# Performance work log

Hardware: AMD Instinct MI355X
Metric: run time of the kernel (lower is better)

The kernel has to match this reference:

```python
import jax, jax.numpy as jnp
import numpy as np

B, N = 16, 128
DN0, DE0, DH = 64, 16, 128  # input node dim, input edge dim, hidden dim


def _gnn2(A, x, e, w_msg, b_msg, w_node, b_node):
    """One GNN2 layer on dense batched graphs.
    A: [B,N,N] adjacency mask, x: [B,N,Dn], e: [B,N,N,De].
    Message/new-edge: relu(Linear([x_i, x_j, e_ij])) masked by A.
    New node: relu(Linear([x, sum_j msg_ij])).
    The concat-Linear is decomposed into three matmuls to avoid
    materializing the [B,N,N,2Dn+De] concat tensor.
    """
    Dn = x.shape[-1]
    Wi, Wj, We = w_msg[:Dn], w_msg[Dn:2 * Dn], w_msg[2 * Dn:]
    xi = x @ Wi                                   # [B,N,Do]
    xj = x @ Wj                                   # [B,N,Do]
    msg = jax.nn.relu(xi[:, :, None, :] + xj[:, None, :, :] + e @ We + b_msg)
    msg = msg * A[..., None]                      # mask non-edges -> new edge_attr [B,N,N,Do]
    agg = msg.sum(axis=2)                         # scatter-sum over neighbors j -> [B,N,Do]
    Wx, Wa = w_node[:Dn], w_node[Dn:]
    x_new = jax.nn.relu(x @ Wx + agg @ Wa + b_node)
    return x_new, msg


def setup_inputs() -> dict:
    key = jax.random.key(0)
    ks = iter(jax.random.split(key, 32))
    s = 0.05
    inp = {
        "edge_index": jax.random.randint(next(ks), (B, N, N), 0, 2, dtype=jnp.int32),
        "x": jax.random.normal(next(ks), (B, N, DN0), dtype=jnp.float32),
        "edge_attr": jax.random.normal(next(ks), (B, N, N, DE0), dtype=jnp.float32),
    }
    def w(shape):
        return s * jax.random.normal(next(ks), shape, dtype=jnp.float32)
    # layer 0: node_in=64, edge_in=16 -> 128
    inp["w_msg_0"], inp["b_msg_0"] = w((2 * DN0 + DE0, DH)), w((DH,))
    inp["w_node_0"], inp["b_node_0"] = w((DN0 + DH, DH)), w((DH,))
    # layers 1,2: 128 -> 128
    for l in (1, 2):
        inp[f"w_msg_{l}"], inp[f"b_msg_{l}"] = w((2 * DH + DH, DH)), w((DH,))
        inp[f"w_node_{l}"], inp[f"b_node_{l}"] = w((DH + DH, DH)), w((DH,))
    # head mlp: 128 -> 128 -> 128 -> 1
    inp["w_h1"], inp["b_h1"] = w((DH, DH)), w((DH,))
    inp["w_h2"], inp["b_h2"] = w((DH, DH)), w((DH,))
    inp["w_h3"], inp["b_h3"] = w((DH, 1)), w((1,))
    return inp


def reference(edge_index, x, edge_attr,
              w_msg_0, b_msg_0, w_node_0, b_node_0,
              w_msg_1, b_msg_1, w_node_1, b_node_1,
              w_msg_2, b_msg_2, w_node_2, b_node_2,
              w_h1, b_h1, w_h2, b_h2, w_h3, b_h3):
    A = edge_index.astype(jnp.float32)
    x = x.astype(jnp.float32)
    # layer 0
    x, e = _gnn2(A, x, edge_attr, w_msg_0, b_msg_0, w_node_0, b_node_0)
    # middle layer with 0.5 residual blend
    x_, e_ = _gnn2(A, x, e, w_msg_1, b_msg_1, w_node_1, b_node_1)
    x = 0.5 * (x + x_)
    e = 0.5 * (e + e_)
    # last layer
    x, e = _gnn2(A, x, e, w_msg_2, b_msg_2, w_node_2, b_node_2)
    # edge_mean readout + MLP head
    h = e.mean(axis=(1, 2))                       # [B, DH]
    h = jax.nn.relu(h @ w_h1 + b_h1)
    h = jax.nn.relu(h @ w_h2 + b_h2)
    out = h @ w_h3 + b_h3                         # [B, 1]
    return out.squeeze(-1)                        # [B]
```

## Files before the change

kernel.cpp:

```cpp
#include <hip/hip_runtime.h>

constexpr int B = 16, N = 128, D = 128, DN0 = 64, DE0 = 16;

typedef _Float16 half8 __attribute__((ext_vector_type(8)));
typedef _Float16 half4 __attribute__((ext_vector_type(4)));
typedef float floatx4 __attribute__((ext_vector_type(4)));

__device__ __forceinline__ void gld16(const _Float16* g, _Float16* l) {
  __builtin_amdgcn_global_load_lds(
      (const __attribute__((address_space(1))) void*)g,
      (__attribute__((address_space(3))) void*)l, 16, 0, 0);
}

__global__ __launch_bounds__(128) void k_wprep(
    const float* __restrict__ wm1, const float* __restrict__ wm2,
    _Float16* __restrict__ weT1, _Float16* __restrict__ weT2) {
  const int bid = blockIdx.x;
  const int layer = bid >> 7, c = bid & 127;
  const int k = threadIdx.x;
  const float* src = layer ? wm2 : wm1;
  _Float16* dst = layer ? weT2 : weT1;
  dst[c * D + k] = (_Float16)src[(2 * D + k) * D + c];
}

__global__ __launch_bounds__(128) void k_pre0(
    const float* __restrict__ x, const float* __restrict__ wm0,
    const float* __restrict__ bm0,
    float* __restrict__ xi0, float* __restrict__ xj0) {
  const int row = blockIdx.x;
  const int c = threadIdx.x;
  __shared__ float xr[DN0];
  if (c < DN0) xr[c] = x[row * DN0 + c];
  __syncthreads();
  float ai = bm0[c], aj = 0.f;
  #pragma unroll 8
  for (int k = 0; k < DN0; ++k) {
    const float xv = xr[k];
    ai = fmaf(xv, wm0[k * D + c], ai);
    aj = fmaf(xv, wm0[(DN0 + k) * D + c], aj);
  }
  xi0[row * D + c] = ai;
  xj0[row * D + c] = aj;
}

__global__ __launch_bounds__(256) void k_edge0(
    const int* __restrict__ ei, const float* __restrict__ eattr,
    const float* __restrict__ wm0,
    const float* __restrict__ xi0, const float* __restrict__ xj0,
    _Float16* __restrict__ msg0, float* __restrict__ agg0) {
  const int row = blockIdx.x;
  const int b = row >> 7;
  const int t = threadIdx.x;
  const int c4 = (t & 31) * 4, jb = t >> 5;

  __shared__ float e_row[N][20];
  __shared__ float w_t[DE0][D];
  __shared__ float amask[N];
  __shared__ float xi_r[D];
  __shared__ float hp2[8][32][4];

  const float4* esrc = (const float4*)(eattr + (size_t)row * N * DE0);
  const float4* wsrc = (const float4*)(wm0 + 2 * DN0 * D);
  #pragma unroll
  for (int u = 0; u < 2; ++u) {
    const int idx4 = u * 256 + t;
    const int j = idx4 >> 2;
    const int k4 = (idx4 & 3) * 4;
    *(float4*)&e_row[j][k4] = esrc[idx4];
    ((float4*)&w_t[0][0])[idx4] = wsrc[idx4];
  }
  if (t < N) {
    amask[t] = (float)ei[(size_t)row * N + t];
    xi_r[t] = xi0[row * D + t];
  }
  __syncthreads();

  float acc[16][4] = {};
  #pragma unroll 4
  for (int k = 0; k < DE0; ++k) {
    float av[16];
    #pragma unroll
    for (int p = 0; p < 16; ++p) av[p] = e_row[jb + 8 * p][k];
    const floatx4 wv = *(const floatx4*)&w_t[k][c4];
    #pragma unroll
    for (int p = 0; p < 16; ++p)
      #pragma unroll
      for (int q = 0; q < 4; ++q)
        acc[p][q] = fmaf(av[p], wv[q], acc[p][q]);
  }

  float hq[4] = {};
  const float* xjb = xj0 + (size_t)b * N * D;
  _Float16* mrow = msg0 + (size_t)row * N * D;
  const floatx4 xiv = *(const floatx4*)&xi_r[c4];
  #pragma unroll
  for (int p = 0; p < 16; ++p) {
    const int j = jb + 8 * p;
    const float am = amask[j];
    const floatx4 xjv = *(const floatx4*)&xjb[j * D + c4];
    half4 hv;
    #pragma unroll
    for (int q = 0; q < 4; ++q) {
      float v = xiv[q] + xjv[q] + acc[p][q];
      v = fmaxf(v, 0.f) * am;
      hv[q] = (_Float16)v;
      hq[q] += v;
    }
    const int cell = (c4 >> 3) ^ (j & 15);
    *(half4*)&mrow[j * D + cell * 8 + (c4 & 7)] = hv;
  }
  #pragma unroll
  for (int q = 0; q < 4; ++q) hp2[jb][t & 31][q] = hq[q];
  __syncthreads();
  if (t < D) {
    float s = 0.f;
    #pragma unroll
    for (int g = 0; g < 8; ++g) s += hp2[g][t >> 2][t & 3];
    agg0[row * D + t] = s;
  }
}

__global__ __launch_bounds__(128) void k_node0(
    const float* __restrict__ x0, const float* __restrict__ agg0,
    const float* __restrict__ wn0, const float* __restrict__ bn0,
    const float* __restrict__ wm1, const float* __restrict__ bm1,
    float* __restrict__ x1, float* __restrict__ xi1, float* __restrict__ xj1) {
  const int row = blockIdx.x;
  const int c = threadIdx.x;
  __shared__ float xr[DN0], ar[D], x1r[D];
  if (c < DN0) xr[c] = x0[row * DN0 + c];
  ar[c] = agg0[row * D + c];
  __syncthreads();
  float a = bn0[c];
  #pragma unroll 8
  for (int k = 0; k < DN0; ++k) a = fmaf(xr[k], wn0[k * D + c], a);
  #pragma unroll 8
  for (int k = 0; k < D; ++k) a = fmaf(ar[k], wn0[(DN0 + k) * D + c], a);
  a = fmaxf(a, 0.f);
  x1[row * D + c] = a;
  x1r[c] = a;
  __syncthreads();
  float ai = bm1[c], aj = 0.f;
  #pragma unroll 8
  for (int k = 0; k < D; ++k) {
    const float xv = x1r[k];
    ai = fmaf(xv, wm1[k * D + c], ai);
    aj = fmaf(xv, wm1[(D + k) * D + c], aj);
  }
  xi1[row * D + c] = ai;
  xj1[row * D + c] = aj;
}

__global__ __launch_bounds__(128) void k_node1(
    const float* __restrict__ x1, const float* __restrict__ agg1,
    const float* __restrict__ wn1, const float* __restrict__ bn1,
    const float* __restrict__ wm2, const float* __restrict__ bm2,
    float* __restrict__ xi2, float* __restrict__ xj2) {
  const int row = blockIdx.x;
  const int c = threadIdx.x;
  __shared__ float x1r[D], ar[D], x2r[D];
  x1r[c] = x1[row * D + c];
  ar[c] = agg1[row * D + c];
  __syncthreads();
  float a = bn1[c];
  #pragma unroll 8
  for (int k = 0; k < D; ++k) a = fmaf(x1r[k], wn1[k * D + c], a);
  #pragma unroll 8
  for (int k = 0; k < D; ++k) a = fmaf(ar[k], wn1[(D + k) * D + c], a);
  x2r[c] = 0.5f * (x1r[c] + fmaxf(a, 0.f));
  __syncthreads();
  float ai = bm2[c], aj = 0.f;
  #pragma unroll 8
  for (int k = 0; k < D; ++k) {
    const float xv = x2r[k];
    ai = fmaf(xv, wm2[k * D + c], ai);
    aj = fmaf(xv, wm2[(D + k) * D + c], aj);
  }
  xi2[row * D + c] = ai;
  xj2[row * D + c] = aj;
}

__global__ __launch_bounds__(512, 4) void k_mid(
    const int* __restrict__ ei, const _Float16* __restrict__ weT1,
    const _Float16* __restrict__ weT2,
    const float* __restrict__ xi, const float* __restrict__ xj,
    _Float16* __restrict__ em,
    float* __restrict__ agg1) {
  const int row = blockIdx.x;
  const int b = row >> 7;
  const int t = threadIdx.x;
  const int w = t >> 6;
  const int lane = t & 63;
  const int lm = lane & 15, lq = lane >> 4;

  __shared__ _Float16 sE[N * D];

  half8 a1[4];
  #pragma unroll
  for (int ks = 0; ks < 4; ++ks)
    a1[ks] = *(const half8*)(weT1 + (16 * w + lm) * D + 8 * lq + 32 * ks);

  const _Float16* gsrc = em + (size_t)row * N * D;
  #pragma unroll
  for (int u = 0; u < 4; ++u) {
    const int seg = (u * 8 + w) * 512;
    gld16(gsrc + seg + lane * 8, &sE[seg]);
  }

  const int c0 = 16 * w + 4 * lq;
  const floatx4 xiv = *(const floatx4*)&xi[(size_t)row * D + c0];
  float am[8];
  #pragma unroll
  for (int jt = 0; jt < 8; ++jt)
    am[jt] = (float)ei[(size_t)row * N + 16 * jt + lm];

  __syncthreads();

  floatx4 acc[8];
  #pragma unroll
  for (int jt = 0; jt < 8; ++jt) acc[jt] = (floatx4){0.f, 0.f, 0.f, 0.f};
  #pragma unroll
  for (int ks = 0; ks < 4; ++ks)
    #pragma unroll
    for (int jt = 0; jt < 8; ++jt) {
      const half8 bv = *(const half8*)&sE[(16 * jt + lm) * D + (((lq + 4 * ks) ^ lm) << 3)];
      acc[jt] = __builtin_amdgcn_mfma_f32_16x16x32_f16(a1[ks], bv, acc[jt], 0, 0, 0);
    }

  __syncthreads();

  const float* xjb = xj + (size_t)b * N * D;
  floatx4 hacc = (floatx4){0.f, 0.f, 0.f, 0.f};
  #pragma unroll
  for (int jt = 0; jt < 8; ++jt) {
    const int j = 16 * jt + lm;
    const int hidx = j * D + (((2 * w + (lq >> 1)) ^ lm) << 3) + 4 * (lq & 1);
    const floatx4 xjv = *(const floatx4*)&xjb[j * D + c0];
    const half4 m0 = *(const half4*)&sE[hidx];
    half4 mid;
    floatx4 m1;
    #pragma unroll
    for (int r = 0; r < 4; ++r) {
      const float v = xiv[r] + xjv[r] + acc[jt][r];
      m1[r] = fmaxf(v, 0.f) * am[jt];
      mid[r] = (_Float16)(0.5f * ((float)m0[r] + m1[r]));
    }
    *(half4*)&sE[hidx] = mid;
    hacc += m1;
  }

  half8 a2[4];
  #pragma unroll
  for (int ks = 0; ks < 4; ++ks)
    a2[ks] = *(const half8*)(weT2 + (16 * w + lm) * D + 8 * lq + 32 * ks);

  __syncthreads();

  #pragma unroll
  for (int jt = 0; jt < 8; ++jt) acc[jt] = (floatx4){0.f, 0.f, 0.f, 0.f};
  #pragma unroll
  for (int ks = 0; ks < 4; ++ks)
    #pragma unroll
    for (int jt = 0; jt < 8; ++jt) {
      const half8 bv = *(const half8*)&sE[(16 * jt + lm) * D + (((lq + 4 * ks) ^ lm) << 3)];
      acc[jt] = __builtin_amdgcn_mfma_f32_16x16x32_f16(a2[ks], bv, acc[jt], 0, 0, 0);
    }

  #pragma unroll
  for (int m = 1; m < 16; m <<= 1)
    #pragma unroll
    for (int r = 0; r < 4; ++r)
      hacc[r] += __shfl_xor(hacc[r], m, 64);
  if (lm == 0)
    *(floatx4*)&agg1[(size_t)row * D + c0] = hacc;

  __syncthreads();

  #pragma unroll
  for (int jt = 0; jt < 8; ++jt) {
    const int j = 16 * jt + lm;
    const int hidx = j * D + (((2 * w + (lq >> 1)) ^ lm) << 3) + 4 * (lq & 1);
    half4 tv;
    #pragma unroll
    for (int r = 0; r < 4; ++r) tv[r] = (_Float16)acc[jt][r];
    *(half4*)&sE[hidx] = tv;
  }

  __syncthreads();

  uint4* gdst = (uint4*)(em + (size_t)row * N * D);
  const uint4* ls = (const uint4*)sE;
  #pragma unroll
  for (int u = 0; u < 4; ++u) {
    const int idx4 = (u * 8 + w) * 64 + lane;
    gdst[idx4] = ls[idx4];
  }
}

__global__ __launch_bounds__(256) void k_fin(
    const int* __restrict__ ei, const _Float16* __restrict__ t2,
    const float* __restrict__ xi, const float* __restrict__ xj,
    float* __restrict__ rowsum) {
  const int row = blockIdx.x;
  const int b = row >> 7;
  const int t = threadIdx.x;
  const int c8 = (t & 15) * 8, jr = t >> 4;

  __shared__ float sMask[N];
  __shared__ float hp[16][16][8];
  if (t < N) sMask[t] = (float)ei[(size_t)row * N + t];
  float xiv[8];
  *(floatx4*)&xiv[0] = *(const floatx4*)&xi[row * D + c8];
  *(floatx4*)&xiv[4] = *(const floatx4*)&xi[row * D + c8 + 4];
  __syncthreads();

  const _Float16* src = t2 + (size_t)row * N * D;
  const float* xjb = xj + (size_t)b * N * D;
  float acc8[8] = {};
  #pragma unroll
  for (int u = 0; u < 8; ++u) {
    const int j = u * 16 + jr;
    const half8 tv = *(const half8*)(src + j * D + (((t & 15) ^ jr) << 3));
    const float am = sMask[j];
    const floatx4 xj0 = *(const floatx4*)&xjb[j * D + c8];
    const floatx4 xj1 = *(const floatx4*)&xjb[j * D + c8 + 4];
    #pragma unroll
    for (int r = 0; r < 4; ++r) {
      acc8[r]     += fmaxf(xiv[r] + xj0[r] + (float)tv[r], 0.f) * am;
      acc8[4 + r] += fmaxf(xiv[4 + r] + xj1[r] + (float)tv[4 + r], 0.f) * am;
    }
  }
  #pragma unroll
  for (int k = 0; k < 8; ++k) hp[jr][t & 15][k] = acc8[k];
  __syncthreads();
  if (t < D) {
    float s = 0.f;
    #pragma unroll
    for (int g = 0; g < 16; ++g) s += hp[g][t >> 3][t & 7];
    rowsum[row * D + t] = s;
  }
}

__global__ __launch_bounds__(128) void k_head(
    const float* __restrict__ rowsum,
    const float* __restrict__ w1, const float* __restrict__ b1,
    const float* __restrict__ w2, const float* __restrict__ b2,
    const float* __restrict__ w3, const float* __restrict__ b3,
    float* __restrict__ out) {
  const int b = blockIdx.x;
  const int c = threadIdx.x;
  __shared__ float hr[D], h1r[D], h2r[D];
  const float* rs = rowsum + (size_t)b * N * D;
  float s = 0.f;
  for (int i = 0; i < N; ++i) s += rs[i * D + c];
  hr[c] = s * (1.f / (N * N));
  __syncthreads();
  float a = b1[c];
  #pragma unroll 8
  for (int k = 0; k < D; ++k) a = fmaf(hr[k], w1[k * D + c], a);
  h1r[c] = fmaxf(a, 0.f);
  __syncthreads();
  a = b2[c];
  #pragma unroll 8
  for (int k = 0; k < D; ++k) a = fmaf(h1r[k], w2[k * D + c], a);
  h2r[c] = fmaxf(a, 0.f);
  __syncthreads();
  hr[c] = h2r[c] * w3[c];
  __syncthreads();
  if (c == 0) {
    float s2 = b3[0];
    for (int k = 0; k < D; ++k) s2 += hr[k];
    out[b] = s2;
  }
}

extern "C" void kernel_launch(void* const* d_in, const int* in_sizes, int n_in,
                              void* d_out, int out_size, void* d_ws, size_t ws_size,
                              hipStream_t stream) {
  const int*   ei  = (const int*)d_in[0];
  const float* x0  = (const float*)d_in[1];
  const float* ea  = (const float*)d_in[2];
  const float* wm0 = (const float*)d_in[3];
  const float* bm0 = (const float*)d_in[4];
  const float* wn0 = (const float*)d_in[5];
  const float* bn0 = (const float*)d_in[6];
  const float* wm1 = (const float*)d_in[7];
  const float* bm1 = (const float*)d_in[8];
  const float* wn1 = (const float*)d_in[9];
  const float* bn1 = (const float*)d_in[10];
  const float* wm2 = (const float*)d_in[11];
  const float* bm2 = (const float*)d_in[12];
  const float* wh1 = (const float*)d_in[15];
  const float* bh1 = (const float*)d_in[16];
  const float* wh2 = (const float*)d_in[17];
  const float* bh2 = (const float*)d_in[18];
  const float* wh3 = (const float*)d_in[19];
  const float* bh3 = (const float*)d_in[20];
  float* out = (float*)d_out;

  _Float16* msg0h = (_Float16*)d_ws;
  _Float16* weT1  = msg0h + (size_t)B * N * N * D;
  _Float16* weT2  = weT1 + D * D;
  float* f = (float*)(weT2 + D * D);
  size_t off = 0;
  const size_t R = (size_t)B * N * D;
  float* xi0  = f + off; off += R;
  float* xj0  = f + off; off += R;
  float* agg0 = f + off; off += R;
  float* x1   = f + off; off += R;
  float* xi1  = f + off; off += R;
  float* xj1  = f + off; off += R;
  float* agg1 = f + off; off += R;
  float* xi2  = f + off; off += R;
  float* xj2  = f + off; off += R;
  float* rsum = f + off; off += R;

  const int rows = B * N;
  k_wprep<<<256, 128, 0, stream>>>(wm1, wm2, weT1, weT2);
  k_pre0 <<<rows, 128, 0, stream>>>(x0, wm0, bm0, xi0, xj0);
  k_edge0<<<rows, 256, 0, stream>>>(ei, ea, wm0, xi0, xj0, msg0h, agg0);
  k_node0<<<rows, 128, 0, stream>>>(x0, agg0, wn0, bn0, wm1, bm1, x1, xi1, xj1);
  k_mid  <<<rows, 512, 0, stream>>>(ei, weT1, weT2, xi1, xj1, msg0h, agg1);
  k_node1<<<rows, 128, 0, stream>>>(x1, agg1, wn1, bn1, wm2, bm2, xi2, xj2);
  k_fin  <<<rows, 256, 0, stream>>>(ei, msg0h, xi2, xj2, rsum);
  k_head <<<B,    128, 0, stream>>>(rsum, wh1, bh1, wh2, bh2, wh3, bh3, out);
}
```

Baseline: 240.7 us.

## Switch k_mid to 32x32x16 MFMA tiles with 4 waves per block

```diff
diff --git a/kernel.cpp b/kernel.cpp
--- a/kernel.cpp
+++ b/kernel.cpp
@@ -5,6 +5,7 @@
 typedef _Float16 half8 __attribute__((ext_vector_type(8)));
 typedef _Float16 half4 __attribute__((ext_vector_type(4)));
 typedef float floatx4 __attribute__((ext_vector_type(4)));
+typedef float floatx16 __attribute__((ext_vector_type(16)));
 
 __device__ __forceinline__ void gld16(const _Float16* g, _Float16* l) {
   __builtin_amdgcn_global_load_lds(
@@ -180,7 +181,7 @@
   xj2[row * D + c] = aj;
 }
 
-__global__ __launch_bounds__(512, 4) void k_mid(
+__global__ __launch_bounds__(256, 2) void k_mid(
     const int* __restrict__ ei, const _Float16* __restrict__ weT1,
     const _Float16* __restrict__ weT2,
     const float* __restrict__ xi, const float* __restrict__ xj,
@@ -191,99 +192,121 @@
   const int t = threadIdx.x;
   const int w = t >> 6;
   const int lane = t & 63;
-  const int lm = lane & 15, lq = lane >> 4;
+  const int l31 = lane & 31;
+  const int l15 = lane & 15;
+  const int hl = lane >> 5;
 
   __shared__ _Float16 sE[N * D];
 
-  half8 a1[4];
-  #pragma unroll
-  for (int ks = 0; ks < 4; ++ks)
-    a1[ks] = *(const half8*)(weT1 + (16 * w + lm) * D + 8 * lq + 32 * ks);
-
   const _Float16* gsrc = em + (size_t)row * N * D;
   #pragma unroll
-  for (int u = 0; u < 4; ++u) {
-    const int seg = (u * 8 + w) * 512;
+  for (int u = 0; u < 8; ++u) {
+    const int seg = (u * 4 + w) * 512;
     gld16(gsrc + seg + lane * 8, &sE[seg]);
   }
 
-  const int c0 = 16 * w + 4 * lq;
-  const floatx4 xiv = *(const floatx4*)&xi[(size_t)row * D + c0];
-  float am[8];
-  #pragma unroll
-  for (int jt = 0; jt < 8; ++jt)
-    am[jt] = (float)ei[(size_t)row * N + 16 * jt + lm];
-
-  __syncthreads();
-
-  floatx4 acc[8];
-  #pragma unroll
-  for (int jt = 0; jt < 8; ++jt) acc[jt] = (floatx4){0.f, 0.f, 0.f, 0.f};
-  #pragma unroll
-  for (int ks = 0; ks < 4; ++ks)
-    #pragma unroll
-    for (int jt = 0; jt < 8; ++jt) {
-      const half8 bv = *(const half8*)&sE[(16 * jt + lm) * D + (((lq + 4 * ks) ^ lm) << 3)];
-      acc[jt] = __builtin_amdgcn_mfma_f32_16x16x32_f16(a1[ks], bv, acc[jt], 0, 0, 0);
+  half8 a1[8];
+  #pragma unroll
+  for (int ks = 0; ks < 8; ++ks)
+    a1[ks] = *(const half8*)(weT1 + (32 * w + l31) * D + 16 * ks + 8 * hl);
+
+  floatx4 xiv[4];
+  #pragma unroll
+  for (int g = 0; g < 4; ++g)
+    xiv[g] = *(const floatx4*)&xi[(size_t)row * D + 32 * w + 8 * g + 4 * hl];
+  float am[4];
+  #pragma unroll
+  for (int jt = 0; jt < 4; ++jt)
+    am[jt] = (float)ei[(size_t)row * N + 32 * jt + l31];
+
+  __syncthreads();
+
+  const floatx16 vzero = {0.f,0.f,0.f,0.f,0.f,0.f,0.f,0.f,
+                          0.f,0.f,0.f,0.f,0.f,0.f,0.f,0.f};
+  floatx16 acc[4];
+  #pragma unroll
+  for (int jt = 0; jt < 4; ++jt) acc[jt] = vzero;
+  #pragma unroll
+  for (int ks = 0; ks < 8; ++ks)
+    #pragma unroll
+    for (int jt = 0; jt < 4; ++jt) {
+      const half8 bv = *(const half8*)
+          &sE[(32 * jt + l31) * D + (((2 * ks + hl) ^ l15) << 3)];
+      acc[jt] = __builtin_amdgcn_mfma_f32_32x32x16_f16(a1[ks], bv, acc[jt], 0, 0, 0);
     }
 
   __syncthreads();
 
   const float* xjb = xj + (size_t)b * N * D;
-  floatx4 hacc = (floatx4){0.f, 0.f, 0.f, 0.f};
-  #pragma unroll
-  for (int jt = 0; jt < 8; ++jt) {
-    const int j = 16 * jt + lm;
-    const int hidx = j * D + (((2 * w + (lq >> 1)) ^ lm) << 3) + 4 * (lq & 1);
-    const floatx4 xjv = *(const floatx4*)&xjb[j * D + c0];
-    const half4 m0 = *(const half4*)&sE[hidx];
-    half4 mid;
-    floatx4 m1;
-    #pragma unroll
-    for (int r = 0; r < 4; ++r) {
-      const float v = xiv[r] + xjv[r] + acc[jt][r];
-      m1[r] = fmaxf(v, 0.f) * am[jt];
-      mid[r] = (_Float16)(0.5f * ((float)m0[r] + m1[r]));
-    }
-    *(half4*)&sE[hidx] = mid;
-    hacc += m1;
-  }
-
-  half8 a2[4];
-  #pragma unroll
-  for (int ks = 0; ks < 4; ++ks)
-    a2[ks] = *(const half8*)(weT2 + (16 * w + lm) * D + 8 * lq + 32 * ks);
-
-  __syncthreads();
-
-  #pragma unroll
-  for (int jt = 0; jt < 8; ++jt) acc[jt] = (floatx4){0.f, 0.f, 0.f, 0.f};
-  #pragma unroll
-  for (int ks = 0; ks < 4; ++ks)
-    #pragma unroll
-    for (int jt = 0; jt < 8; ++jt) {
-      const half8 bv = *(const half8*)&sE[(16 * jt + lm) * D + (((lq + 4 * ks) ^ lm) << 3)];
-      acc[jt] = __builtin_amdgcn_mfma_f32_16x16x32_f16(a2[ks], bv, acc[jt], 0, 0, 0);
-    }
-
-  #pragma unroll
-  for (int m = 1; m < 16; m <<= 1)
-    #pragma unroll
-    for (int r = 0; r < 4; ++r)
-      hacc[r] += __shfl_xor(hacc[r], m, 64);
-  if (lm == 0)
-    *(floatx4*)&agg1[(size_t)row * D + c0] = hacc;
-
-  __syncthreads();
-
-  #pragma unroll
-  for (int jt = 0; jt < 8; ++jt) {
-    const int j = 16 * jt + lm;
-    const int hidx = j * D + (((2 * w + (lq >> 1)) ^ lm) << 3) + 4 * (lq & 1);
-    half4 tv;
-    #pragma unroll
-    for (int r = 0; r < 4; ++r) tv[r] = (_Float16)acc[jt][r];
-    *(half4*)&sE[hidx] = tv;
+  floatx4 hacc[4];
+  #pragma unroll
+  for (int g = 0; g < 4; ++g) hacc[g] = (floatx4){0.f, 0.f, 0.f, 0.f};
+  #pragma unroll
+  for (int jt = 0; jt < 4; ++jt) {
+    const int j = 32 * jt + l31;
+    #pragma unroll
+    for (int g = 0; g < 4; ++g) {
+      const int cofs = 32 * w + 8 * g + 4 * hl;
+      const int hidx = j * D + (((4 * w + g) ^ l15) << 3) + 4 * hl;
+      const floatx4 xjv = *(const floatx4*)&xjb[j * D + cofs];
+      const half4 m0 = *(const half4*)&sE[hidx];
+      half4 mid;
+      floatx4 m1;
+      #pragma unroll
+      for (int r = 0; r < 4; ++r) {
+        const float v = xiv[g][r] + xjv[r] + acc[jt][4 * g + r];
+        m1[r] = fmaxf(v, 0.f) * am[jt];
+        mid[r] = (_Float16)(0.5f * ((float)m0[r] + m1[r]));
+      }
+      *(half4*)&sE[hidx] = mid;
+      hacc[g] += m1;
+    }
+  }
+
+  #pragma unroll
+  for (int m = 1; m < 32; m <<= 1)
+    #pragma unroll
+    for (int g = 0; g < 4; ++g)
+      #pragma unroll
+      for (int r = 0; r < 4; ++r)
+        hacc[g][r] += __shfl_xor(hacc[g][r], m, 64);
+  if (l31 == 0) {
+    #pragma unroll
+    for (int g = 0; g < 4; ++g)
+      *(floatx4*)&agg1[(size_t)row * D + 32 * w + 8 * g + 4 * hl] = hacc[g];
+  }
+
+  half8 a2[8];
+  #pragma unroll
+  for (int ks = 0; ks < 8; ++ks)
+    a2[ks] = *(const half8*)(weT2 + (32 * w + l31) * D + 16 * ks + 8 * hl);
+
+  __syncthreads();
+
+  #pragma unroll
+  for (int jt = 0; jt < 4; ++jt) acc[jt] = vzero;
+  #pragma unroll
+  for (int ks = 0; ks < 8; ++ks)
+    #pragma unroll
+    for (int jt = 0; jt < 4; ++jt) {
+      const half8 bv = *(const half8*)
+          &sE[(32 * jt + l31) * D + (((2 * ks + hl) ^ l15) << 3)];
+      acc[jt] = __builtin_amdgcn_mfma_f32_32x32x16_f16(a2[ks], bv, acc[jt], 0, 0, 0);
+    }
+
+  __syncthreads();
+
+  #pragma unroll
+  for (int jt = 0; jt < 4; ++jt) {
+    const int j = 32 * jt + l31;
+    #pragma unroll
+    for (int g = 0; g < 4; ++g) {
+      const int hidx = j * D + (((4 * w + g) ^ l15) << 3) + 4 * hl;
+      half4 tv;
+      #pragma unroll
+      for (int r = 0; r < 4; ++r) tv[r] = (_Float16)acc[jt][4 * g + r];
+      *(half4*)&sE[hidx] = tv;
+    }
   }
 
   __syncthreads();
@@ -291,8 +314,8 @@
   uint4* gdst = (uint4*)(em + (size_t)row * N * D);
   const uint4* ls = (const uint4*)sE;
   #pragma unroll
-  for (int u = 0; u < 4; ++u) {
-    const int idx4 = (u * 8 + w) * 64 + lane;
+  for (int u = 0; u < 8; ++u) {
+    const int idx4 = u * 256 + t;
     gdst[idx4] = ls[idx4];
   }
 }
@@ -420,7 +443,7 @@
   k_pre0 <<<rows, 128, 0, stream>>>(x0, wm0, bm0, xi0, xj0);
   k_edge0<<<rows, 256, 0, stream>>>(ei, ea, wm0, xi0, xj0, msg0h, agg0);
   k_node0<<<rows, 128, 0, stream>>>(x0, agg0, wn0, bn0, wm1, bm1, x1, xi1, xj1);
-  k_mid  <<<rows, 512, 0, stream>>>(ei, weT1, weT2, xi1, xj1, msg0h, agg1);
+  k_mid  <<<rows, 256, 0, stream>>>(ei, weT1, weT2, xi1, xj1, msg0h, agg1);
   k_node1<<<rows, 128, 0, stream>>>(x1, agg1, wn1, bn1, wm2, bm2, xi2, xj2);
   k_fin  <<<rows, 256, 0, stream>>>(ei, msg0h, xi2, xj2, rsum);
   k_head <<<B,    128, 0, stream>>>(rsum, wh1, bh1, wh2, bh2, wh3, bh3, out);
```

New measurement: 239.4 us. About the same (-0.5%).
